# Kernel optimization log

Hardware: AMD Instinct MI355X
Metric: run time of the kernel (lower is better)

Reference implementation:

```python
import jax, jax.numpy as jnp
import numpy as np

NEG_SLOPE = 0.1


def setup_inputs() -> dict:
    key = jax.random.key(0)
    k1, k2, k3 = jax.random.split(key, 3)
    l, b, d = 96, 16, 512
    x = jax.random.normal(k1, (l, b, d), dtype=jnp.float32)
    # nn.Linear(2*d, d): weight (d, 2*d), bias (d,)
    W = jax.random.normal(k2, (d, 2 * d), dtype=jnp.float32) * (1.0 / np.sqrt(2 * d))
    bias = jax.random.normal(k3, (d,), dtype=jnp.float32) * 0.01
    return {"x": x, "W": W, "bias": bias}


def reference(x, W, bias):
    """CatLayer forward.
    x: (l, b, c) -> out: (l*l, b, c)
    pair[i, j] = Linear(LeakyReLU(concat(x[i], x[j])))
    """
    l, b, c = x.shape
    # Outer pairwise concat: (l, l, b, 2c); first half is x[i], second half x[j]
    xi = jnp.broadcast_to(x[:, None, :, :], (l, l, b, c))
    xj = jnp.broadcast_to(x[None, :, :, :], (l, l, b, c))
    h = jnp.concatenate([xi, xj], axis=-1)          # (l, l, b, 2c)
    h = jax.nn.leaky_relu(h, negative_slope=NEG_SLOPE)
    out = jnp.einsum('ijbk,ck->ijbc', h, W) + bias  # (l, l, b, c)
    return out.reshape(l * l, b, c)
```

## Files before the change

### kernel.cpp

```cpp
#include <hip/hip_runtime.h>
#include <hip/hip_bf16.h>
#include <stdint.h>


typedef __attribute__((ext_vector_type(8))) short short8;
typedef __attribute__((ext_vector_type(4))) short short4v;
typedef __attribute__((ext_vector_type(4))) float f32x4;

#define L_DIM 96
#define B_DIM 16
#define C_DIM 512
#define M_DIM 1536
#define K_DIM 512
#define N_DIM 1024

__device__ inline unsigned short f32_to_bf16(float f) {
    union { float f; uint32_t u; } c; c.f = f;
    uint32_t u = c.u;
    uint32_t r = (u + 0x7FFFu + ((u >> 16) & 1u)) >> 16;
    return (unsigned short)r;
}

#define LDS_STRIDE 40
__global__ __launch_bounds__(256) void gemm_pq(const float* __restrict__ x,
                                               const float* __restrict__ W,
                                               const float* __restrict__ bias,
                                               float* __restrict__ C) {
    __shared__ unsigned short As[128 * LDS_STRIDE];
    __shared__ unsigned short Bs[128 * LDS_STRIDE];
    const int bm = blockIdx.x;
    const int bn = blockIdx.y;
    const int tid = threadIdx.x;
    const int lane = tid & 63;
    const int w  = tid >> 6;
    const int wr = w >> 1, wc = w & 1;
    const int l15 = lane & 15, l4 = lane >> 4;

    const float* wbase = (bn < 4) ? (W + (size_t)(bn * 128) * N_DIM)
                                  : (W + (size_t)(bn * 128 - C_DIM) * N_DIM + C_DIM);
    const float* xbase = x + (size_t)(bm * 128) * K_DIM;

    f32x4 acc[4][4] = {};

    for (int kt = 0; kt < K_DIM / 32; ++kt) {
        __syncthreads();
#pragma unroll
        for (int r = 0; r < 4; ++r) {
            int chunk = tid + 256 * r;
            int row = chunk >> 3;
            int kc  = (chunk & 7) << 2;
            f32x4 va = *(const f32x4*)(xbase + (size_t)row * K_DIM + kt * 32 + kc);
            short4v sa;
#pragma unroll
            for (int e = 0; e < 4; ++e) {
                float f = va[e];
                f = f > 0.f ? f : 0.1f * f;
                sa[e] = (short)f32_to_bf16(f);
            }
            *(short4v*)(&As[row * LDS_STRIDE + kc]) = sa;
            f32x4 vb = *(const f32x4*)(wbase + (size_t)row * N_DIM + kt * 32 + kc);
            short4v sb;
#pragma unroll
            for (int e = 0; e < 4; ++e) sb[e] = (short)f32_to_bf16(vb[e]);
            *(short4v*)(&Bs[row * LDS_STRIDE + kc]) = sb;
        }
        __syncthreads();
        short8 a[4], b[4];
#pragma unroll
        for (int m = 0; m < 4; ++m)
            a[m] = *(const short8*)(&As[(wr * 64 + m * 16 + l15) * LDS_STRIDE + l4 * 8]);
#pragma unroll
        for (int n = 0; n < 4; ++n)
            b[n] = *(const short8*)(&Bs[(wc * 64 + n * 16 + l15) * LDS_STRIDE + l4 * 8]);
#pragma unroll
        for (int m = 0; m < 4; ++m)
#pragma unroll
            for (int n = 0; n < 4; ++n)
                acc[m][n] = __builtin_amdgcn_mfma_f32_16x16x32_bf16(a[m], b[n], acc[m][n], 0, 0, 0);
    }

#pragma unroll
    for (int m = 0; m < 4; ++m) {
#pragma unroll
        for (int n = 0; n < 4; ++n) {
            int col = bn * 128 + wc * 64 + n * 16 + l15;
            float bv = (col < C_DIM) ? bias[col] : 0.f;
#pragma unroll
            for (int i = 0; i < 4; ++i) {
                int row = bm * 128 + wr * 64 + m * 16 + l4 * 4 + i;
                C[(size_t)row * N_DIM + col] = acc[m][n][i] + bv;
            }
        }
    }
}

__global__ __launch_bounds__(256) void combine_k(const f32x4* __restrict__ PQ,
                                                 f32x4* __restrict__ out) {
    const int jh   = blockIdx.x & 1;
    const int rest = blockIdx.x >> 1;
    const int t    = rest * 256 + threadIdx.x;
    const uint32_t c4 = t & 127u;
    const uint32_t r  = (uint32_t)t >> 7;
    const uint32_t b  = r & 15u;
    const uint32_t i  = r >> 4;

    const f32x4 p = PQ[(size_t)r * 256u + c4];
    const f32x4* qrow = PQ + (size_t)b * 256u + 128u + c4;
    f32x4* orow = out + ((size_t)(i * 96u) * 16u + b) * 128u + c4;

    const int j0 = jh * 48, j1 = j0 + 48;
#pragma unroll 4
    for (int j = j0; j < j1; ++j) {
        f32x4 q = qrow[(size_t)j * 16u * 256u];
        __builtin_nontemporal_store(p + q, orow + (size_t)j * 16u * 128u);
    }
}

extern "C" void kernel_launch(void* const* d_in, const int* in_sizes, int n_in,
                              void* d_out, int out_size, void* d_ws, size_t ws_size,
                              hipStream_t stream) {
    const float* x    = (const float*)d_in[0];
    const float* W    = (const float*)d_in[1];
    const float* bias = (const float*)d_in[2];
    float* out = (float*)d_out;

    float* PQ = (float*)d_ws;

    dim3 g(M_DIM / 128, N_DIM / 128);
    gemm_pq<<<g, 256, 0, stream>>>(x, W, bias, PQ);
    combine_k<<<1536, 256, 0, stream>>>((const f32x4*)PQ, (f32x4*)out);
}
```

Measured before the change: 77.88 us.

## Retile GEMM for more blocks with K-phase LDS staging, split combine into more blocks

The GEMM tile shrinks from 128x128 to 96x64, so the grid grows from 96 to 256 blocks and covers more CUs. The K loop now stages 256-wide K halves in LDS, giving two barrier phases instead of sixteen at the cost of much more LDS per block. The combine kernel splits the j range into 8 chunks of 12 rather than 2 of 48, and loads all q values up front before storing, for more parallelism and memory-level overlap. Larger LDS use may reduce occupancy, and p is now re-read more times.

After: 67.80 us. 12.9% less time.

```diff
diff --git a/kernel.cpp b/kernel.cpp
--- a/kernel.cpp
+++ b/kernel.cpp
@@ -14,6 +14,11 @@
 #define K_DIM 512
 #define N_DIM 1024
 
+#define TM 96
+#define TN 64
+#define KPH 256
+#define ASTR 264
+
 __device__ inline unsigned short f32_to_bf16(float f) {
     union { float f; uint32_t u; } c; c.f = f;
     uint32_t u = c.u;
@@ -21,13 +26,12 @@
     return (unsigned short)r;
 }
 
-#define LDS_STRIDE 40
 __global__ __launch_bounds__(256) void gemm_pq(const float* __restrict__ x,
                                                const float* __restrict__ W,
                                                const float* __restrict__ bias,
                                                float* __restrict__ C) {
-    __shared__ unsigned short As[128 * LDS_STRIDE];
-    __shared__ unsigned short Bs[128 * LDS_STRIDE];
+    __shared__ unsigned short As[TM * ASTR];
+    __shared__ unsigned short Bs[TN * ASTR];
     const int bm = blockIdx.x;
     const int bn = blockIdx.y;
     const int tid = threadIdx.x;
@@ -36,84 +40,93 @@
     const int wr = w >> 1, wc = w & 1;
     const int l15 = lane & 15, l4 = lane >> 4;
 
-    const float* wbase = (bn < 4) ? (W + (size_t)(bn * 128) * N_DIM)
-                                  : (W + (size_t)(bn * 128 - C_DIM) * N_DIM + C_DIM);
-    const float* xbase = x + (size_t)(bm * 128) * K_DIM;
+    const float* xbase = x + (size_t)(bm * TM) * K_DIM;
+    const float* wbase = (bn < 8) ? (W + (size_t)(bn * TN) * N_DIM)
+                                  : (W + (size_t)(bn * TN - C_DIM) * N_DIM + C_DIM);
 
-    f32x4 acc[4][4] = {};
+    f32x4 acc[3][2] = {};
 
-    for (int kt = 0; kt < K_DIM / 32; ++kt) {
+    for (int ph = 0; ph < 2; ++ph) {
+        __syncthreads();
+#pragma unroll 4
+        for (int r = 0; r < 24; ++r) {
+            int q = tid + 256 * r;
+            int row = q >> 6, kc4 = (q & 63) << 2;
+            f32x4 v = *(const f32x4*)(xbase + (size_t)row * K_DIM + ph * KPH + kc4);
+            short4v s;
+#pragma unroll
+            for (int e = 0; e < 4; ++e) {
+                float f = v[e];
+                f = f > 0.f ? f : 0.1f * f;
+                s[e] = (short)f32_to_bf16(f);
+            }
+            *(short4v*)(&As[row * ASTR + kc4]) = s;
+        }
+#pragma unroll 4
+        for (int r = 0; r < 16; ++r) {
+            int q = tid + 256 * r;
+            int row = q >> 6, kc4 = (q & 63) << 2;
+            f32x4 v = *(const f32x4*)(wbase + (size_t)row * N_DIM + ph * KPH + kc4);
+            short4v s;
+#pragma unroll
+            for (int e = 0; e < 4; ++e) s[e] = (short)f32_to_bf16(v[e]);
+            *(short4v*)(&Bs[row * ASTR + kc4]) = s;
+        }
         __syncthreads();
 #pragma unroll
-        for (int r = 0; r < 4; ++r) {
-            int chunk = tid + 256 * r;
-            int row = chunk >> 3;
-            int kc  = (chunk & 7) << 2;
-            f32x4 va = *(const f32x4*)(xbase + (size_t)row * K_DIM + kt * 32 + kc);
-            short4v sa;
+        for (int kt = 0; kt < 8; ++kt) {
+            short8 a[3], b[2];
 #pragma unroll
-            for (int e = 0; e < 4; ++e) {
-                float f = va[e];
-                f = f > 0.f ? f : 0.1f * f;
-                sa[e] = (short)f32_to_bf16(f);
-            }
-            *(short4v*)(&As[row * LDS_STRIDE + kc]) = sa;
-            f32x4 vb = *(const f32x4*)(wbase + (size_t)row * N_DIM + kt * 32 + kc);
-            short4v sb;
+            for (int m = 0; m < 3; ++m)
+                a[m] = *(const short8*)(&As[(wr * 48 + m * 16 + l15) * ASTR + kt * 32 + l4 * 8]);
 #pragma unroll
-            for (int e = 0; e < 4; ++e) sb[e] = (short)f32_to_bf16(vb[e]);
-            *(short4v*)(&Bs[row * LDS_STRIDE + kc]) = sb;
+            for (int n = 0; n < 2; ++n)
+                b[n] = *(const short8*)(&Bs[(wc * 32 + n * 16 + l15) * ASTR + kt * 32 + l4 * 8]);
+#pragma unroll
+            for (int m = 0; m < 3; ++m)
+#pragma unroll
+                for (int n = 0; n < 2; ++n)
+                    acc[m][n] = __builtin_amdgcn_mfma_f32_16x16x32_bf16(a[m], b[n], acc[m][n], 0, 0, 0);
         }
-        __syncthreads();
-        short8 a[4], b[4];
-#pragma unroll
-        for (int m = 0; m < 4; ++m)
-            a[m] = *(const short8*)(&As[(wr * 64 + m * 16 + l15) * LDS_STRIDE + l4 * 8]);
-#pragma unroll
-        for (int n = 0; n < 4; ++n)
-            b[n] = *(const short8*)(&Bs[(wc * 64 + n * 16 + l15) * LDS_STRIDE + l4 * 8]);
-#pragma unroll
-        for (int m = 0; m < 4; ++m)
-#pragma unroll
-            for (int n = 0; n < 4; ++n)
-                acc[m][n] = __builtin_amdgcn_mfma_f32_16x16x32_bf16(a[m], b[n], acc[m][n], 0, 0, 0);
     }
 
 #pragma unroll
-    for (int m = 0; m < 4; ++m) {
+    for (int m = 0; m < 3; ++m) {
 #pragma unroll
-        for (int n = 0; n < 4; ++n) {
-            int col = bn * 128 + wc * 64 + n * 16 + l15;
-            float bv = (col < C_DIM) ? bias[col] : 0.f;
+        for (int n = 0; n < 2; ++n) {
+            int col = bn * TN + wc * 32 + n * 16 + l15;
+            float bv = (bn < 8) ? bias[col] : 0.f;
 #pragma unroll
-            for (int i = 0; i < 4; ++i) {
-                int row = bm * 128 + wr * 64 + m * 16 + l4 * 4 + i;
-                C[(size_t)row * N_DIM + col] = acc[m][n][i] + bv;
+            for (int e = 0; e < 4; ++e) {
+                int row = bm * TM + wr * 48 + m * 16 + l4 * 4 + e;
+                C[(size_t)row * N_DIM + col] = acc[m][n][e] + bv;
             }
         }
     }
 }
 
-__global__ __launch_bounds__(256) void combine_k(const f32x4* __restrict__ PQ,
-                                                 f32x4* __restrict__ out) {
-    const int jh   = blockIdx.x & 1;
-    const int rest = blockIdx.x >> 1;
-    const int t    = rest * 256 + threadIdx.x;
-    const uint32_t c4 = t & 127u;
-    const uint32_t r  = (uint32_t)t >> 7;
-    const uint32_t b  = r & 15u;
-    const uint32_t i  = r >> 4;
+__global__ __launch_bounds__(256) void combine_k(const f32x4* __restrict__ PQ4,
+                                                 f32x4* __restrict__ out4) {
+    const int jh   = blockIdx.x & 7;
+    const int rest = blockIdx.x >> 3;
+    const int g    = rest * 256 + threadIdx.x;
+    const uint32_t c4 = (uint32_t)g & 127u;
+    const uint32_t rg = (uint32_t)g >> 7;
+    const uint32_t b  = rg & 15u;
+    const uint32_t i  = rg >> 4;
 
-    const f32x4 p = PQ[(size_t)r * 256u + c4];
-    const f32x4* qrow = PQ + (size_t)b * 256u + 128u + c4;
-    f32x4* orow = out + ((size_t)(i * 96u) * 16u + b) * 128u + c4;
+    const f32x4 p = PQ4[(size_t)rg * 256u + c4];
+    const int j0 = jh * 12;
+    const f32x4* qb = PQ4 + ((size_t)(j0 * 16u + b)) * 256u + 128u + c4;
 
-    const int j0 = jh * 48, j1 = j0 + 48;
-#pragma unroll 4
-    for (int j = j0; j < j1; ++j) {
-        f32x4 q = qrow[(size_t)j * 16u * 256u];
-        __builtin_nontemporal_store(p + q, orow + (size_t)j * 16u * 128u);
-    }
+    f32x4 q[12];
+#pragma unroll
+    for (int j = 0; j < 12; ++j) q[j] = qb[(size_t)j * 4096u];
+
+    f32x4* ob = out4 + ((size_t)(i * 96u + (uint32_t)j0) * 16u + b) * 128u + c4;
+#pragma unroll
+    for (int j = 0; j < 12; ++j)
+        __builtin_nontemporal_store(p + q[j], ob + (size_t)j * 2048u);
 }
 
 extern "C" void kernel_launch(void* const* d_in, const int* in_sizes, int n_in,
@@ -126,7 +139,7 @@
 
     float* PQ = (float*)d_ws;
 
-    dim3 g(M_DIM / 128, N_DIM / 128);
+    dim3 g(M_DIM / TM, N_DIM / TN);
     gemm_pq<<<g, 256, 0, stream>>>(x, W, bias, PQ);
-    combine_k<<<1536, 256, 0, stream>>>((const f32x4*)PQ, (f32x4*)out);
+    combine_k<<<6144, 256, 0, stream>>>((const f32x4*)PQ, (f32x4*)out);
 }
```
